# Performance work log

Hardware: AMD Instinct MI355X
Metric: run time of the kernel (lower is better)

The kernel has to match this reference:

```python
import jax, jax.numpy as jnp
import numpy as np


def setup_inputs() -> dict:
    key = jax.random.key(0)
    ks = jax.random.split(key, 7)
    B, S, D, H, Dh = 4, 2048, 1024, 16, 64
    return {
        "query_input": jax.random.normal(ks[0], (B, S, D), jnp.float32),
        "key_input": jax.random.normal(ks[1], (B, S, D), jnp.float32),
        "value_input": jax.random.normal(ks[2], (B, S, D), jnp.float32),
        "Wq": jax.random.normal(ks[3], (D, H, Dh), jnp.float32) * 0.03,
        "Wk": jax.random.normal(ks[4], (D, H, Dh), jnp.float32) * 0.03,
        "Wv": jax.random.normal(ks[5], (D, H, Dh), jnp.float32) * 0.03,
        "Wo": jax.random.normal(ks[6], (H, Dh, D), jnp.float32) * 0.03,
    }


def reference(query_input, key_input, value_input, Wq, Wk, Wv, Wo):
    # Projections: [B,S,D] x [D,H,Dh] -> [B,S,H,Dh]
    q = jnp.einsum("bsd,dhk->bshk", query_input, Wq)
    k = jnp.einsum("bsd,dhk->bshk", key_input, Wk)
    v = jnp.einsum("bsd,dhk->bshk", value_input, Wv)
    depth = Wq.shape[-1]
    q = q * (depth ** -0.5)
    # logits: [B,H,F,T]  (F = query len, T = key len)
    logits = jnp.einsum("bthk,bfhk->bhft", k, q)
    weights = jax.nn.softmax(logits, axis=-1)
    # attention output: [B,F,H,Dh]
    ctx = jnp.einsum("bhft,bthk->bfhk", weights, v)
    # output projection: [B,F,H,Dh] x [H,Dh,D] -> [B,F,D]
    return jnp.einsum("bfhk,hkd->bfd", ctx, Wo)
```

## Files before the change

kernel.cpp:

```cpp
#include <hip/hip_runtime.h>
#include <stdint.h>

typedef __bf16 bf16;
typedef __bf16 bf16x4 __attribute__((ext_vector_type(4)));
typedef __bf16 bf16x8 __attribute__((ext_vector_type(8)));
typedef float f32x4 __attribute__((ext_vector_type(4)));
typedef float f32x16 __attribute__((ext_vector_type(16)));

#define AS1 __attribute__((address_space(1)))
#define AS3 __attribute__((address_space(3)))

__device__ __forceinline__ void async16(void* lds, const void* g) {
    __builtin_amdgcn_global_load_lds((AS1 void*)g, (AS3 void*)lds, 16, 0, 0);
}

__global__ __launch_bounds__(256) void prep(
    const float* __restrict__ x0, const float* __restrict__ x1,
    const float* __restrict__ x2,
    bf16* __restrict__ y0, bf16* __restrict__ y1, bf16* __restrict__ y2,
    const float* __restrict__ s0, const float* __restrict__ s1,
    const float* __restrict__ s2, const float* __restrict__ s3,
    bf16* __restrict__ d0, bf16* __restrict__ d1,
    bf16* __restrict__ d2, bf16* __restrict__ d3) {
    const int z = blockIdx.z;
    const int t = threadIdx.x;
    if (z < 3) {
        const float* x = z == 0 ? x0 : z == 1 ? x1 : x2;
        bf16* y = z == 0 ? y0 : z == 1 ? y1 : y2;
        int i = (blockIdx.x * 256 + t) * 8;
        f32x4 a = *(const f32x4*)(x + i);
        f32x4 b = *(const f32x4*)(x + i + 4);
        bf16x8 o;
#pragma unroll
        for (int j = 0; j < 4; ++j) { o[j] = (bf16)a[j]; o[4 + j] = (bf16)b[j]; }
        *(bf16x8*)(y + i) = o;
        return;
    }
    const int bx = blockIdx.x;
    if (bx >= 1024) return;
    const int wsel = bx >> 8, tile = bx & 255;
    const float* W = wsel == 0 ? s0 : wsel == 1 ? s1 : wsel == 2 ? s2 : s3;
    bf16* Wt = wsel == 0 ? d0 : wsel == 1 ? d1 : wsel == 2 ? d2 : d3;
    const int k0 = (tile >> 4) * 64, n0 = (tile & 15) * 64;
    __shared__ float Ts[64 * 65];
    const int c = t & 63, r0 = t >> 6;
#pragma unroll
    for (int i = 0; i < 16; ++i) {
        int r = r0 + i * 4;
        Ts[r * 65 + c] = W[(size_t)(k0 + r) * 1024 + n0 + c];
    }
    __syncthreads();
#pragma unroll
    for (int i = 0; i < 16; ++i) {
        int r = r0 + i * 4;
        Wt[(size_t)(n0 + r) * 1024 + k0 + c] = (bf16)Ts[c * 65 + r];
    }
}

template <typename OutT>
__device__ __forceinline__ void gemm_body(const bf16* __restrict__ A,
                                          const bf16* __restrict__ Bt,
                                          OutT* __restrict__ C,
                                          int N, int K, float scale,
                                          int m0, int n0,
                                          bf16* As, bf16* Bs) {
    const int t = threadIdx.x;
    const int lane = t & 63;
    const int w = t >> 6;
    const int l15 = lane & 15;
    const int quad = lane >> 4;
    const int wm = w >> 1, wn = w & 1;

    f32x4 acc[4][4];
#pragma unroll
    for (int i = 0; i < 4; ++i)
#pragma unroll
        for (int j = 0; j < 4; ++j) acc[i][j] = (f32x4){0.f, 0.f, 0.f, 0.f};

    const bf16* gA[4];
    const bf16* gB[4];
#pragma unroll
    for (int j = 0; j < 4; ++j) {
        int c = j * 256 + t;
        int row = c >> 3, g = (c & 7) ^ (row & 7);
        gA[j] = A + (size_t)(m0 + row) * K + g * 8;
        gB[j] = Bt + (size_t)(n0 + row) * K + g * 8;
    }

    for (int k0 = 0; k0 < K; k0 += 64) {
        __syncthreads();
#pragma unroll
        for (int j = 0; j < 4; ++j) {
            async16(As + (j * 256 + w * 64) * 8, gA[j] + k0);
            async16(Bs + (j * 256 + w * 64) * 8, gB[j] + k0);
        }
        __syncthreads();
#pragma unroll
        for (int kk = 0; kk < 2; ++kk) {
            bf16x8 af[4], bfv[4];
#pragma unroll
            for (int mi = 0; mi < 4; ++mi) {
                int r = wm * 64 + mi * 16 + l15;
                af[mi] = *(const bf16x8*)&As[r * 64 + (((kk * 4 + quad) ^ (r & 7)) * 8)];
            }
#pragma unroll
            for (int ni = 0; ni < 4; ++ni) {
                int r = wn * 64 + ni * 16 + l15;
                bfv[ni] = *(const bf16x8*)&Bs[r * 64 + (((kk * 4 + quad) ^ (r & 7)) * 8)];
            }
#pragma unroll
            for (int mi = 0; mi < 4; ++mi)
#pragma unroll
                for (int ni = 0; ni < 4; ++ni)
                    acc[mi][ni] = __builtin_amdgcn_mfma_f32_16x16x32_bf16(
                        af[mi], bfv[ni], acc[mi][ni], 0, 0, 0);
        }
    }

#pragma unroll
    for (int mi = 0; mi < 4; ++mi)
#pragma unroll
        for (int ni = 0; ni < 4; ++ni)
#pragma unroll
            for (int r = 0; r < 4; ++r) {
                int row = m0 + wm * 64 + mi * 16 + quad * 4 + r;
                int col = n0 + wn * 64 + ni * 16 + l15;
                C[(size_t)row * N + col] = (OutT)(acc[mi][ni][r] * scale);
            }
}

__global__ __launch_bounds__(256) void gemm_qkv(
    const bf16* __restrict__ Xq, const bf16* __restrict__ Xk, const bf16* __restrict__ Xv,
    const bf16* __restrict__ Wqt, const bf16* __restrict__ Wkt, const bf16* __restrict__ Wvt,
    bf16* __restrict__ Qb, bf16* __restrict__ Kb, bf16* __restrict__ VtG) {
    __shared__ __align__(16) bf16 As[128 * 64];
    __shared__ __align__(16) bf16 Bs[128 * 64];
    const int z = blockIdx.z;
    const int blk = blockIdx.x;
    const int big  = (blk & 7) * 8 + (blk >> 6);
    const int sml  = (blk >> 3) & 7;
    const bf16* A; const bf16* Bt; bf16* C; int N; float scale; int m0, n0;
    if (z == 0) { A = Xq; Bt = Wqt; C = Qb; N = 1024; scale = 0.18033688011112042f;
                  m0 = big * 128; n0 = sml * 128; }
    else if (z == 1) { A = Xk; Bt = Wkt; C = Kb; N = 1024; scale = 1.0f;
                  m0 = big * 128; n0 = sml * 128; }
    else { A = Wvt; Bt = Xv; C = VtG; N = 8192; scale = 1.0f;
                  m0 = sml * 128; n0 = big * 128; }
    gemm_body<bf16>(A, Bt, C, N, 1024, scale, m0, n0, As, Bs);
}

__global__ __launch_bounds__(256) void gemm_out(const bf16* __restrict__ A,
                                                const bf16* __restrict__ Bt,
                                                float* __restrict__ C) {
    __shared__ __align__(16) bf16 As[128 * 64];
    __shared__ __align__(16) bf16 Bs[128 * 64];
    const int blk = blockIdx.x;
    const int big = (blk & 7) * 8 + (blk >> 6);
    const int sml = (blk >> 3) & 7;
    gemm_body<float>(A, Bt, C, 1024, 1024, 1.0f, big * 128, sml * 128, As, Bs);
}

__global__ __launch_bounds__(256, 2) void attn_fa(const bf16* __restrict__ Q,
                                                  const bf16* __restrict__ K,
                                                  const bf16* __restrict__ Vt,
                                                  bf16* __restrict__ O) {
    __shared__ __align__(16) bf16 Ks[2][64 * 64];
    __shared__ __align__(16) bf16 Vs[2][64 * 64];
    __shared__ __align__(16) bf16 Ps[4][64 * 64];

    const int t = threadIdx.x;
    const int lane = t & 63;
    const int w = t >> 6;
    const int l31 = lane & 31;
    const int h = lane >> 5;

    const int bid = blockIdx.x;
    const int bh = (bid & 7) * 8 + ((bid >> 3) & 7);
    const int q0 = (bid >> 6) * 256;
    const int b = bh >> 4, hh = bh & 15;
    const size_t baseQ = (size_t)b * 2048 * 1024 + (size_t)hh * 64;

    const int r0s = t >> 3,          g0s = (t & 7) ^ (r0s & 7);
    const int r1s = (t + 256) >> 3,  g1s = ((t + 256) & 7) ^ (r1s & 7);
    const bf16* gK0 = K + baseQ + (size_t)r0s * 1024 + g0s * 8;
    const bf16* gK1 = K + baseQ + (size_t)r1s * 1024 + g1s * 8;
    const bf16* gV0 = Vt + (size_t)(hh * 64 + r0s) * 8192 + (size_t)b * 2048 + g0s * 8;
    const bf16* gV1 = Vt + (size_t)(hh * 64 + r1s) * 8192 + (size_t)b * 2048 + g1s * 8;

    bf16x8 qf[2][4];
#pragma unroll
    for (int Qt = 0; Qt < 2; ++Qt)
#pragma unroll
        for (int c = 0; c < 4; ++c)
            qf[Qt][c] = *(const bf16x8*)(Q + baseQ +
                (size_t)(q0 + w * 64 + Qt * 32 + l31) * 1024 + c * 16 + h * 8);

    f32x16 accO[2][2];
    float l_part[2] = {0.f, 0.f};
#pragma unroll
    for (int dt = 0; dt < 2; ++dt)
#pragma unroll
        for (int Qt = 0; Qt < 2; ++Qt)
#pragma unroll
            for (int r = 0; r < 16; ++r) accO[dt][Qt][r] = 0.f;

    auto stage = [&](int t0, int bi) {
        async16((bf16*)Ks[bi] + w * 512,        gK0 + (size_t)t0 * 1024);
        async16((bf16*)Ks[bi] + 2048 + w * 512, gK1 + (size_t)t0 * 1024);
        async16((bf16*)Vs[bi] + w * 512,        gV0 + t0);
        async16((bf16*)Vs[bi] + 2048 + w * 512, gV1 + t0);
    };

    stage(0, 0);
    bf16* Pp = &Ps[w][0];

    for (int it = 0; it < 32; ++it) {
        __syncthreads();
        if (it + 1 < 32) stage((it + 1) * 64, (it + 1) & 1);
        const bf16* Kb = Ks[it & 1];
        const bf16* Vb = Vs[it & 1];

        f32x16 accS[2][2];
#pragma unroll
        for (int T = 0; T < 2; ++T)
#pragma unroll
            for (int Qt = 0; Qt < 2; ++Qt)
#pragma unroll
                for (int r = 0; r < 16; ++r) accS[T][Qt][r] = 0.f;
#pragma unroll
        for (int c = 0; c < 4; ++c) {
            bf16x8 kf[2];
#pragma unroll
            for (int T = 0; T < 2; ++T) {
                int tr = T * 32 + l31;
                kf[T] = *(const bf16x8*)&Kb[tr * 64 + (((c * 2 + h) ^ (tr & 7)) * 8)];
            }
            __builtin_amdgcn_s_setprio(1);
#pragma unroll
            for (int T = 0; T < 2; ++T)
#pragma unroll
                for (int Qt = 0; Qt < 2; ++Qt)
                    accS[T][Qt] = __builtin_amdgcn_mfma_f32_32x32x16_bf16(
                        kf[T], qf[Qt][c], accS[T][Qt], 0, 0, 0);
            __builtin_amdgcn_s_setprio(0);
        }

#pragma unroll
        for (int Qt = 0; Qt < 2; ++Qt) {
            const int ql = Qt * 32 + l31;
            const int qbase = ql * 64;
            float rs = 0.f;
#pragma unroll
            for (int T = 0; T < 2; ++T)
#pragma unroll
                for (int g = 0; g < 4; ++g) {
                    bf16x4 pk;
#pragma unroll
                    for (int o = 0; o < 4; ++o) {
                        float p = __builtin_amdgcn_exp2f(accS[T][Qt][g * 4 + o]);
                        rs += p;
                        pk[o] = (bf16)p;
                    }
                    int tg = T * 4 + g;
                    *(bf16x4*)&Pp[qbase + ((tg ^ (ql & 7)) * 8) + h * 4] = pk;
                }
            l_part[Qt] += rs;
        }

#pragma unroll
        for (int c = 0; c < 4; ++c) {
            bf16x8 vf[2], pf[2];
#pragma unroll
            for (int dt = 0; dt < 2; ++dt) {
                int dh = dt * 32 + l31;
                vf[dt] = *(const bf16x8*)&Vb[dh * 64 + (((c * 2 + h) ^ (dh & 7)) * 8)];
            }
#pragma unroll
            for (int Qt = 0; Qt < 2; ++Qt) {
                int ql = Qt * 32 + l31;
                int tg = c * 2 + h;
                pf[Qt] = *(const bf16x8*)&Pp[ql * 64 + ((tg ^ (ql & 7)) * 8)];
            }
            __builtin_amdgcn_s_setprio(1);
#pragma unroll
            for (int dt = 0; dt < 2; ++dt)
#pragma unroll
                for (int Qt = 0; Qt < 2; ++Qt)
                    accO[dt][Qt] = __builtin_amdgcn_mfma_f32_32x32x16_bf16(
                        vf[dt], pf[Qt], accO[dt][Qt], 0, 0, 0);
            __builtin_amdgcn_s_setprio(0);
        }
    }

    float inv[2];
#pragma unroll
    for (int Qt = 0; Qt < 2; ++Qt) {
        float l = l_part[Qt];
        l += __shfl_xor(l, 32);
        inv[Qt] = 1.0f / l;
    }

#pragma unroll
    for (int Qt = 0; Qt < 2; ++Qt) {
        size_t rowoff = baseQ + (size_t)(q0 + w * 64 + Qt * 32 + l31) * 1024;
#pragma unroll
        for (int dt = 0; dt < 2; ++dt)
#pragma unroll
            for (int g = 0; g < 4; ++g) {
                bf16x4 o;
#pragma unroll
                for (int r = 0; r < 4; ++r)
                    o[r] = (bf16)(accO[dt][Qt][g * 4 + r] * inv[Qt]);
                *(bf16x4*)&O[rowoff + dt * 32 + g * 8 + h * 4] = o;
            }
    }
}

extern "C" void kernel_launch(void* const* d_in, const int* in_sizes, int n_in,
                              void* d_out, int out_size, void* d_ws, size_t ws_size,
                              hipStream_t stream) {
    const float* qin = (const float*)d_in[0];
    const float* kin = (const float*)d_in[1];
    const float* vin = (const float*)d_in[2];
    const float* Wq = (const float*)d_in[3];
    const float* Wk = (const float*)d_in[4];
    const float* Wv = (const float*)d_in[5];
    const float* Wo = (const float*)d_in[6];
    float* out = (float*)d_out;

    char* ws = (char*)d_ws;
    bf16* Xq  = (bf16*)(ws);
    bf16* Xk  = (bf16*)(ws + ((size_t)16 << 20));
    bf16* Xv  = (bf16*)(ws + ((size_t)32 << 20));
    bf16* Qb  = (bf16*)(ws + ((size_t)48 << 20));
    bf16* Kb  = (bf16*)(ws + ((size_t)64 << 20));
    bf16* VtG = (bf16*)(ws + ((size_t)80 << 20));
    bf16* Cb  = (bf16*)(ws);
    bf16* Wqt = (bf16*)(ws + ((size_t)96 << 20));
    bf16* Wkt = Wqt + 1024 * 1024;
    bf16* Wvt = Wkt + 1024 * 1024;
    bf16* Wot = Wvt + 1024 * 1024;

    prep<<<dim3(4096, 1, 4), 256, 0, stream>>>(qin, kin, vin, Xq, Xk, Xv,
                                               Wq, Wk, Wv, Wo, Wqt, Wkt, Wvt, Wot);
    gemm_qkv<<<dim3(512, 1, 3), 256, 0, stream>>>(Xq, Xk, Xv, Wqt, Wkt, Wvt,
                                                  Qb, Kb, VtG);
    attn_fa<<<dim3(512), 256, 0, stream>>>(Qb, Kb, VtG, Cb);
    gemm_out<<<dim3(512), 256, 0, stream>>>(Cb, Wot, out);
}
```

Measured before the change: 314.8 us.

## Keep attention P in registers via permlane32 swap, use 8 waves of 32 rows

The attention kernel no longer writes softmax probabilities to shared memory and reads them back. It rearranges the bf16-packed P values across half-waves with v_permlane32_swap so the S accumulator layout matches the B operand of the PV MFMA. Each wave now handles 32 query rows instead of 64, and the block grows to 512 threads with launch bounds of 4, so each staging step needs one async load per thread. This removes the LDS round-trip and its bank traffic, lowers register pressure and raises occupancy. The cost is half the K/V fragment reuse per wave, so LDS reads of K and V per MFMA double.

```diff
diff --git a/kernel.cpp b/kernel.cpp
--- a/kernel.cpp
+++ b/kernel.cpp
@@ -160,13 +160,18 @@
     gemm_body<float>(A, Bt, C, 1024, 1024, 1.0f, big * 128, sml * 128, As, Bs);
 }
 
-__global__ __launch_bounds__(256, 2) void attn_fa(const bf16* __restrict__ Q,
+__device__ __forceinline__ uint32_t pk2(float a, float b) {
+    union { bf16 h[2]; uint32_t u; } x;
+    x.h[0] = (bf16)a; x.h[1] = (bf16)b;
+    return x.u;
+}
+
+__global__ __launch_bounds__(512, 4) void attn_fa(const bf16* __restrict__ Q,
                                                   const bf16* __restrict__ K,
                                                   const bf16* __restrict__ Vt,
                                                   bf16* __restrict__ O) {
     __shared__ __align__(16) bf16 Ks[2][64 * 64];
     __shared__ __align__(16) bf16 Vs[2][64 * 64];
-    __shared__ __align__(16) bf16 Ps[4][64 * 64];
 
     const int t = threadIdx.x;
     const int lane = t & 63;
@@ -180,39 +185,29 @@
     const int b = bh >> 4, hh = bh & 15;
     const size_t baseQ = (size_t)b * 2048 * 1024 + (size_t)hh * 64;
 
-    const int r0s = t >> 3,          g0s = (t & 7) ^ (r0s & 7);
-    const int r1s = (t + 256) >> 3,  g1s = ((t + 256) & 7) ^ (r1s & 7);
+    const int r0s = t >> 3, g0s = (t & 7) ^ (r0s & 7);
     const bf16* gK0 = K + baseQ + (size_t)r0s * 1024 + g0s * 8;
-    const bf16* gK1 = K + baseQ + (size_t)r1s * 1024 + g1s * 8;
     const bf16* gV0 = Vt + (size_t)(hh * 64 + r0s) * 8192 + (size_t)b * 2048 + g0s * 8;
-    const bf16* gV1 = Vt + (size_t)(hh * 64 + r1s) * 8192 + (size_t)b * 2048 + g1s * 8;
-
-    bf16x8 qf[2][4];
-#pragma unroll
-    for (int Qt = 0; Qt < 2; ++Qt)
-#pragma unroll
-        for (int c = 0; c < 4; ++c)
-            qf[Qt][c] = *(const bf16x8*)(Q + baseQ +
-                (size_t)(q0 + w * 64 + Qt * 32 + l31) * 1024 + c * 16 + h * 8);
-
-    f32x16 accO[2][2];
-    float l_part[2] = {0.f, 0.f};
+
+    bf16x8 qf[4];
+#pragma unroll
+    for (int c = 0; c < 4; ++c)
+        qf[c] = *(const bf16x8*)(Q + baseQ +
+            (size_t)(q0 + w * 32 + l31) * 1024 + c * 16 + h * 8);
+
+    f32x16 accO[2];
+    float l_part = 0.f;
 #pragma unroll
     for (int dt = 0; dt < 2; ++dt)
 #pragma unroll
-        for (int Qt = 0; Qt < 2; ++Qt)
-#pragma unroll
-            for (int r = 0; r < 16; ++r) accO[dt][Qt][r] = 0.f;
+        for (int r = 0; r < 16; ++r) accO[dt][r] = 0.f;
 
     auto stage = [&](int t0, int bi) {
-        async16((bf16*)Ks[bi] + w * 512,        gK0 + (size_t)t0 * 1024);
-        async16((bf16*)Ks[bi] + 2048 + w * 512, gK1 + (size_t)t0 * 1024);
-        async16((bf16*)Vs[bi] + w * 512,        gV0 + t0);
-        async16((bf16*)Vs[bi] + 2048 + w * 512, gV1 + t0);
+        async16((bf16*)Ks[bi] + w * 512, gK0 + (size_t)t0 * 1024);
+        async16((bf16*)Vs[bi] + w * 512, gV0 + t0);
     };
 
     stage(0, 0);
-    bf16* Pp = &Ps[w][0];
 
     for (int it = 0; it < 32; ++it) {
         __syncthreads();
@@ -220,13 +215,11 @@
         const bf16* Kb = Ks[it & 1];
         const bf16* Vb = Vs[it & 1];
 
-        f32x16 accS[2][2];
+        f32x16 accS[2];
 #pragma unroll
         for (int T = 0; T < 2; ++T)
 #pragma unroll
-            for (int Qt = 0; Qt < 2; ++Qt)
-#pragma unroll
-                for (int r = 0; r < 16; ++r) accS[T][Qt][r] = 0.f;
+            for (int r = 0; r < 16; ++r) accS[T][r] = 0.f;
 #pragma unroll
         for (int c = 0; c < 4; ++c) {
             bf16x8 kf[2];
@@ -238,82 +231,71 @@
             __builtin_amdgcn_s_setprio(1);
 #pragma unroll
             for (int T = 0; T < 2; ++T)
-#pragma unroll
-                for (int Qt = 0; Qt < 2; ++Qt)
-                    accS[T][Qt] = __builtin_amdgcn_mfma_f32_32x32x16_bf16(
-                        kf[T], qf[Qt][c], accS[T][Qt], 0, 0, 0);
+                accS[T] = __builtin_amdgcn_mfma_f32_32x32x16_bf16(
+                    kf[T], qf[c], accS[T], 0, 0, 0);
             __builtin_amdgcn_s_setprio(0);
         }
 
-#pragma unroll
-        for (int Qt = 0; Qt < 2; ++Qt) {
-            const int ql = Qt * 32 + l31;
-            const int qbase = ql * 64;
-            float rs = 0.f;
-#pragma unroll
-            for (int T = 0; T < 2; ++T)
-#pragma unroll
-                for (int g = 0; g < 4; ++g) {
-                    bf16x4 pk;
-#pragma unroll
-                    for (int o = 0; o < 4; ++o) {
-                        float p = __builtin_amdgcn_exp2f(accS[T][Qt][g * 4 + o]);
-                        rs += p;
-                        pk[o] = (bf16)p;
-                    }
-                    int tg = T * 4 + g;
-                    *(bf16x4*)&Pp[qbase + ((tg ^ (ql & 7)) * 8) + h * 4] = pk;
-                }
-            l_part[Qt] += rs;
-        }
+        uint32_t pw[16];
+        float rs = 0.f;
+#pragma unroll
+        for (int T = 0; T < 2; ++T) {
+            float p[16];
+#pragma unroll
+            for (int r = 0; r < 16; ++r) {
+                p[r] = __builtin_amdgcn_exp2f(accS[T][r]);
+                rs += p[r];
+            }
+            uint32_t X0 = pk2(p[0], p[1]),   X1 = pk2(p[2], p[3]);
+            uint32_t Y0 = pk2(p[4], p[5]),   Y1 = pk2(p[6], p[7]);
+            uint32_t X2 = pk2(p[8], p[9]),   X3 = pk2(p[10], p[11]);
+            uint32_t Y2 = pk2(p[12], p[13]), Y3 = pk2(p[14], p[15]);
+            asm volatile("v_permlane32_swap_b32 %0, %1" : "+v"(X0), "+v"(Y0));
+            asm volatile("v_permlane32_swap_b32 %0, %1" : "+v"(X1), "+v"(Y1));
+            asm volatile("v_permlane32_swap_b32 %0, %1" : "+v"(X2), "+v"(Y2));
+            asm volatile("v_permlane32_swap_b32 %0, %1" : "+v"(X3), "+v"(Y3));
+            pw[T * 8 + 0] = X0; pw[T * 8 + 1] = X1;
+            pw[T * 8 + 2] = Y0; pw[T * 8 + 3] = Y1;
+            pw[T * 8 + 4] = X2; pw[T * 8 + 5] = X3;
+            pw[T * 8 + 6] = Y2; pw[T * 8 + 7] = Y3;
+        }
+        l_part += rs;
 
 #pragma unroll
         for (int c = 0; c < 4; ++c) {
-            bf16x8 vf[2], pf[2];
+            bf16x8 vf[2];
 #pragma unroll
             for (int dt = 0; dt < 2; ++dt) {
                 int dh = dt * 32 + l31;
                 vf[dt] = *(const bf16x8*)&Vb[dh * 64 + (((c * 2 + h) ^ (dh & 7)) * 8)];
             }
-#pragma unroll
-            for (int Qt = 0; Qt < 2; ++Qt) {
-                int ql = Qt * 32 + l31;
-                int tg = c * 2 + h;
-                pf[Qt] = *(const bf16x8*)&Pp[ql * 64 + ((tg ^ (ql & 7)) * 8)];
-            }
+            union { uint32_t u[4]; bf16x8 v; } pf;
+#pragma unroll
+            for (int k = 0; k < 4; ++k)
+                pf.u[k] = pw[(c >> 1) * 8 + (c & 1) * 4 + k];
             __builtin_amdgcn_s_setprio(1);
 #pragma unroll
             for (int dt = 0; dt < 2; ++dt)
-#pragma unroll
-                for (int Qt = 0; Qt < 2; ++Qt)
-                    accO[dt][Qt] = __builtin_amdgcn_mfma_f32_32x32x16_bf16(
-                        vf[dt], pf[Qt], accO[dt][Qt], 0, 0, 0);
+                accO[dt] = __builtin_amdgcn_mfma_f32_32x32x16_bf16(
+                    vf[dt], pf.v, accO[dt], 0, 0, 0);
             __builtin_amdgcn_s_setprio(0);
         }
     }
 
-    float inv[2];
-#pragma unroll
-    for (int Qt = 0; Qt < 2; ++Qt) {
-        float l = l_part[Qt];
-        l += __shfl_xor(l, 32);
-        inv[Qt] = 1.0f / l;
-    }
-
-#pragma unroll
-    for (int Qt = 0; Qt < 2; ++Qt) {
-        size_t rowoff = baseQ + (size_t)(q0 + w * 64 + Qt * 32 + l31) * 1024;
-#pragma unroll
-        for (int dt = 0; dt < 2; ++dt)
-#pragma unroll
-            for (int g = 0; g < 4; ++g) {
-                bf16x4 o;
-#pragma unroll
-                for (int r = 0; r < 4; ++r)
-                    o[r] = (bf16)(accO[dt][Qt][g * 4 + r] * inv[Qt]);
-                *(bf16x4*)&O[rowoff + dt * 32 + g * 8 + h * 4] = o;
-            }
-    }
+    float l = l_part + __shfl_xor(l_part, 32);
+    float inv = 1.0f / l;
+
+    size_t rowoff = baseQ + (size_t)(q0 + w * 32 + l31) * 1024;
+#pragma unroll
+    for (int dt = 0; dt < 2; ++dt)
+#pragma unroll
+        for (int g = 0; g < 4; ++g) {
+            bf16x4 o;
+#pragma unroll
+            for (int r = 0; r < 4; ++r)
+                o[r] = (bf16)(accO[dt][g * 4 + r] * inv);
+            *(bf16x4*)&O[rowoff + dt * 32 + g * 8 + h * 4] = o;
+        }
 }
 
 extern "C" void kernel_launch(void* const* d_in, const int* in_sizes, int n_in,
@@ -345,6 +327,6 @@
                                                Wq, Wk, Wv, Wo, Wqt, Wkt, Wvt, Wot);
     gemm_qkv<<<dim3(512, 1, 3), 256, 0, stream>>>(Xq, Xk, Xv, Wqt, Wkt, Wvt,
                                                   Qb, Kb, VtG);
-    attn_fa<<<dim3(512), 256, 0, stream>>>(Qb, Kb, VtG, Cb);
+    attn_fa<<<dim3(512), 512, 0, stream>>>(Qb, Kb, VtG, Cb);
     gemm_out<<<dim3(512), 256, 0, stream>>>(Cb, Wot, out);
 }
```

Result: slower. 321.8 us (+2.2%).
